# Kernel optimization log

Hardware: AMD Instinct MI355X
Metric: run time of the kernel (lower is better)

## Reference

```python
import jax, jax.numpy as jnp
import numpy as np

VOCAB, EMB = 50000, 300
HID, FCH = 128, 64
B, T = 1024, 200


def setup_inputs() -> dict:
    key = jax.random.key(0)
    ks = jax.random.split(key, 10)
    s = 0.05
    return {
        "x": jax.random.randint(ks[0], (B, T), 0, VOCAB),
        "emb_table": jax.random.normal(ks[1], (VOCAB, EMB), jnp.float32) * s,
        "w_ih": jax.random.normal(ks[2], (4 * HID, EMB), jnp.float32) * s,
        "w_hh": jax.random.normal(ks[3], (4 * HID, HID), jnp.float32) * s,
        "b_ih": jax.random.normal(ks[4], (4 * HID,), jnp.float32) * s,
        "b_hh": jax.random.normal(ks[5], (4 * HID,), jnp.float32) * s,
        "fc1_w": jax.random.normal(ks[6], (FCH, HID), jnp.float32) * s,
        "fc1_b": jax.random.normal(ks[7], (FCH,), jnp.float32) * s,
        "fc2_w": jax.random.normal(ks[8], (1, FCH), jnp.float32) * s,
        "fc2_b": jax.random.normal(ks[9], (1,), jnp.float32) * s,
    }


def _lstm_last_h(e, w_ih, w_hh, b_ih, b_hh):
    # e: [B, T, E] -> final hidden state [B, H]
    b, t, _ = e.shape
    h_dim = w_hh.shape[1]
    # Precompute input projections for all timesteps: [T, B, 4H]
    xg = jnp.einsum('bte,ge->tbg', e, w_ih) + (b_ih + b_hh)

    def step(carry, xg_t):
        h, c = carry
        gates = xg_t + h @ w_hh.T  # [B, 4H]
        i, f, g, o = jnp.split(gates, 4, axis=-1)  # PyTorch gate order i,f,g,o
        i = jax.nn.sigmoid(i)
        f = jax.nn.sigmoid(f)
        g = jnp.tanh(g)
        o = jax.nn.sigmoid(o)
        c = f * c + i * g
        h = o * jnp.tanh(c)
        return (h, c), None

    h0 = jnp.zeros((b, h_dim), e.dtype)
    c0 = jnp.zeros((b, h_dim), e.dtype)
    (h_n, _), _ = jax.lax.scan(step, (h0, c0), xg)
    return h_n


def reference(x, emb_table, w_ih, w_hh, b_ih, b_hh, fc1_w, fc1_b, fc2_w, fc2_b):
    e = emb_table[x]  # [B, T, E]
    hn = _lstm_last_h(e, w_ih, w_hh, b_ih, b_hh)  # [B, H]
    # dropout is identity in eval mode
    h1 = jax.nn.relu(hn @ fc1_w.T + fc1_b)  # [B, FCH]
    logits = h1 @ fc2_w.T + fc2_b  # [B, 1]
    return jax.nn.sigmoid(logits)
```

## Files before the change

### kernel.cpp

```cpp
#include <hip/hip_runtime.h>
#include <hip/hip_bf16.h>
#include <stdint.h>

#define VOCAB 50000
#define EMB   300
#define EMBP  320
#define HID   128
#define NGATE 512
#define BATCH 1024
#define SEQ   200
#define ROWS  4
#define L2E   1.4426950408889634f

typedef __attribute__((ext_vector_type(8))) short short8;
typedef __attribute__((ext_vector_type(4))) float f32x4;

#define AS1 __attribute__((address_space(1)))
#define AS3 __attribute__((address_space(3)))

static __device__ __forceinline__ void gload_lds16(const void* g, void* s) {
  __builtin_amdgcn_global_load_lds((const AS1 uint32_t*)g, (AS3 uint32_t*)s, 16, 0, 0);
}

static __device__ __forceinline__ unsigned short f2bf(float f) {
  union { float f; unsigned u; } v; v.f = f;
  unsigned r = v.u + 0x7fffu + ((v.u >> 16) & 1u);
  return (unsigned short)(r >> 16);
}
static __device__ __forceinline__ float blo2f(unsigned u) {
  union { unsigned u; float f; } v; v.u = u << 16; return v.f;
}
static __device__ __forceinline__ float bhi2f(unsigned u) {
  union { unsigned u; float f; } v; v.u = u & 0xffff0000u; return v.f;
}
static __device__ __forceinline__ float sigmf(float x) {
  return __fdividef(1.0f, 1.0f + __expf(-x));
}
static __device__ __forceinline__ float sig2(float z) {
  return __builtin_amdgcn_rcpf(1.0f + __builtin_amdgcn_exp2f(-z));
}

__global__ void k_cvt_pad(const float* __restrict__ src, unsigned short* __restrict__ dst,
                          int rows, int sc, int dc, int perm, int smode) {
  int idx = blockIdx.x * blockDim.x + threadIdx.x;
  int cpr = dc >> 3;
  if (idx >= rows * cpr) return;
  int row = idx / cpr, k0 = (idx - row * cpr) * 8;
  float s = 1.0f;
  if (smode) s = ((row >> 7) == 2) ? (2.0f * L2E) : L2E;
  uint4 pack;
  unsigned short* v = (unsigned short*)&pack;
#pragma unroll
  for (int j = 0; j < 8; j++) {
    int k = k0 + j;
    v[j] = (k < sc) ? f2bf(src[(long)row * sc + k] * s) : (unsigned short)0;
  }
  int drow = perm ? ((row & 127) * 4 + (row >> 7)) : row;
  *(uint4*)(dst + (long)drow * dc + k0) = pack;
}

__global__ void k_bias(const float* __restrict__ a, const float* __restrict__ b,
                       float* __restrict__ o) {
  int i = blockIdx.x * blockDim.x + threadIdx.x;
  if (i < NGATE) {
    int g = i >> 7, hid = i & 127;
    float s = (g == 2) ? (2.0f * L2E) : L2E;
    o[hid * 4 + g] = (a[i] + b[i]) * s;
  }
}

__global__ __launch_bounds__(256) void k_xg_gemm(
    const int* __restrict__ x, const unsigned short* __restrict__ embb,
    const unsigned short* __restrict__ wihb, const float* __restrict__ biasp,
    unsigned short* __restrict__ xg) {
  __shared__ __align__(16) unsigned short Al[128 * 64];
  __shared__ __align__(16) unsigned short Bl[128 * 64];
  const int tid = threadIdx.x;
  const int lane = tid & 63;
  const int tile_n = blockIdx.x & 3, tile_m = blockIdx.x >> 2;
  const int t_idx = tile_m >> 3;
  const int b0 = (tile_m & 7) * 128;
  const int n0 = tile_n * 128;

  const int r0 = tid >> 3;
  const int sg = (tid & 7) ^ (r0 & 7);
  const unsigned short* asrc[4];
  const unsigned short* bsrc[4];
#pragma unroll
  for (int i = 0; i < 4; i++) {
    const int r = r0 + i * 32;
    const long ridx = x[(b0 + r) * SEQ + t_idx];
    asrc[i] = embb + ridx * EMBP + sg * 8;
    bsrc[i] = wihb + (long)(n0 + r) * EMBP + sg * 8;
  }

  const int wid = tid >> 6;
  const int wrow = wid >> 1, wcol = wid & 1;
  const char* Ar = (const char*)Al + (wrow * 64) * 128;
  const char* Br = (const char*)Bl + (wcol * 64) * 128;
  const int l15 = lane & 15, lgrp = lane >> 4;
  const int swz = (l15 & 7) << 4;

  f32x4 acc[4][4];
#pragma unroll
  for (int mt = 0; mt < 4; mt++)
#pragma unroll
    for (int nt = 0; nt < 4; nt++) acc[mt][nt] = (f32x4){0.f, 0.f, 0.f, 0.f};

  for (int ks = 0; ks < EMBP / 64; ks++) {
#pragma unroll
    for (int i = 0; i < 4; i++) {
      gload_lds16(asrc[i] + ks * 64, (char*)Al + tid * 16 + i * 4096);
      gload_lds16(bsrc[i] + ks * 64, (char*)Bl + tid * 16 + i * 4096);
    }
    __syncthreads();
#pragma unroll
    for (int kt = 0; kt < 2; kt++) {
      short8 af[4], bf[4];
#pragma unroll
      for (int mt = 0; mt < 4; mt++)
        af[mt] = *(const short8*)(Ar + (mt * 16 + l15) * 128 + ((kt * 64 + lgrp * 16) ^ swz));
#pragma unroll
      for (int nt = 0; nt < 4; nt++)
        bf[nt] = *(const short8*)(Br + (nt * 16 + l15) * 128 + ((kt * 64 + lgrp * 16) ^ swz));
#pragma unroll
      for (int mt = 0; mt < 4; mt++)
#pragma unroll
        for (int nt = 0; nt < 4; nt++)
          acc[mt][nt] = __builtin_amdgcn_mfma_f32_16x16x32_bf16(af[mt], bf[nt], acc[mt][nt], 0, 0, 0);
    }
    __syncthreads();
  }

  const int m_base = tile_m * 128 + wrow * 64;
  const int colg = n0 + wcol * 64 + l15;
  const int rsub = lgrp * 4;
  float bv[4];
#pragma unroll
  for (int nt = 0; nt < 4; nt++) bv[nt] = biasp[colg + nt * 16];
#pragma unroll
  for (int mt = 0; mt < 4; mt++)
#pragma unroll
    for (int nt = 0; nt < 4; nt++)
#pragma unroll
      for (int j = 0; j < 4; j++) {
        const long m = m_base + mt * 16 + rsub + j;
        xg[m * NGATE + colg + nt * 16] = f2bf(acc[mt][nt][j] + bv[nt]);
      }
}

__global__ __launch_bounds__(512, 2) void k_lstm(
    const unsigned short* __restrict__ xg, const unsigned short* __restrict__ whhb,
    float* __restrict__ hfin) {
  __shared__ __align__(16) unsigned short h_lds[2 * 4 * 128];
  __shared__ __align__(16) float scratch[8 * 256];
  const int tid = threadIdx.x;
  const int lane = tid & 63;
  const int wid = tid >> 6;
  const int b0 = blockIdx.x * ROWS;
  const int l15 = lane & 15;
  const int lgrp = lane >> 4;
  const int hid = wid * 16 + l15;

  short8 bfr[4][4];
#pragma unroll
  for (int g = 0; g < 4; g++)
#pragma unroll
    for (int kt = 0; kt < 4; kt++)
      bfr[g][kt] = *(const short8*)(whhb + (g * 128 + hid) * HID + kt * 32 + lgrp * 8);

  float* sw = scratch + wid * 256;

  float c_r = 0.0f, h_r = 0.0f;

  if (tid < 128) ((uint4*)h_lds)[tid] = make_uint4(0, 0, 0, 0);
  __syncthreads();

  const int ar = l15 & 3;
  int rdoff[4];
#pragma unroll
  for (int kt = 0; kt < 4; kt++)
    rdoff[kt] = ar * 256 + ((kt * 64 + lgrp * 16) ^ (ar << 5));
  const int hwoff = lgrp * 256 + ((2 * hid) ^ (lgrp << 5));
  const char* lb = (const char*)h_lds;

  const unsigned short* xbase = xg + ((long)(b0 + lgrp) * HID + hid) * 4;
  const long TSTEP = (long)BATCH * HID * 4;
  uint2 xA = *(const uint2*)xbase;
  uint2 xB = *(const uint2*)(xbase + TSTEP);
  const unsigned short* xnext = xbase + 2 * TSTEP;

#define STEP_BODY(XS, RB, WB, T)                                               \
  {                                                                            \
    short8 af[4];                                                              \
    _Pragma("unroll") for (int kt = 0; kt < 4; kt++)                           \
      af[kt] = *(const short8*)(lb + (RB) + rdoff[kt]);                        \
    f32x4 acc[4];                                                              \
    _Pragma("unroll") for (int g = 0; g < 4; g++)                              \
      acc[g] = (f32x4){0.f, 0.f, 0.f, 0.f};                                    \
    _Pragma("unroll") for (int kt = 0; kt < 4; kt++)                           \
      _Pragma("unroll") for (int g = 0; g < 4; g++)                            \
        acc[g] = __builtin_amdgcn_mfma_f32_16x16x32_bf16(af[kt], bfr[g][kt],   \
                                                         acc[g], 0, 0, 0);     \
    if (lane < 16) {                                                           \
      _Pragma("unroll") for (int g = 0; g < 4; g++)                            \
        *(f32x4*)(sw + g * 64 + lane * 4) = acc[g];                            \
    }                                                                          \
    asm volatile("s_waitcnt lgkmcnt(0)" ::: "memory");                         \
    const float xf0 = blo2f(XS.x), xf1 = bhi2f(XS.x);                          \
    const float xf2 = blo2f(XS.y), xf3 = bhi2f(XS.y);                          \
    if ((T) + 2 < SEQ) XS = *(const uint2*)xnext;                              \
    const float zi = sw[0 * 64 + l15 * 4 + lgrp] + xf0;                        \
    const float zf = sw[1 * 64 + l15 * 4 + lgrp] + xf1;                        \
    const float zg = sw[2 * 64 + l15 * 4 + lgrp] + xf2;                        \
    const float zo = sw[3 * 64 + l15 * 4 + lgrp] + xf3;                        \
    const float iv = sig2(zi);                                                 \
    const float fv = sig2(zf);                                                 \
    const float gv = 2.0f * sig2(zg) - 1.0f;                                   \
    const float ov = sig2(zo);                                                 \
    c_r = fv * c_r + iv * gv;                                                  \
    const float tc = 2.0f * sig2(c_r * (2.0f * L2E)) - 1.0f;                   \
    h_r = ov * tc;                                                             \
    *(unsigned short*)((char*)h_lds + (WB) + hwoff) = f2bf(h_r);               \
    asm volatile("s_waitcnt lgkmcnt(0)" ::: "memory");                         \
    __builtin_amdgcn_s_barrier();                                              \
    __builtin_amdgcn_sched_barrier(0);                                         \
  }

  for (int t = 0; t < SEQ; t += 2) {
    STEP_BODY(xA, 0, 1024, t);
    xnext += TSTEP;
    STEP_BODY(xB, 1024, 0, t + 1);
    xnext += TSTEP;
  }
#undef STEP_BODY

  hfin[(b0 + lgrp) * HID + hid] = h_r;
}

__global__ void k_head(const float* __restrict__ hfin,
                       const float* __restrict__ fc1w, const float* __restrict__ fc1b,
                       const float* __restrict__ fc2w, const float* __restrict__ fc2b,
                       float* __restrict__ out) {
  const int tid = threadIdx.x;
  const int lane = tid & 63;
  const int wid = tid >> 6;
  const int row = blockIdx.x * 4 + wid;
  const float* h = hfin + row * HID;
  const float* w = fc1w + lane * HID;
  float acc = 0.0f;
#pragma unroll
  for (int k = 0; k < HID; k += 4) {
    const f32x4 hv = *(const f32x4*)(h + k);
    const f32x4 wv = *(const f32x4*)(w + k);
    acc += hv[0] * wv[0] + hv[1] * wv[1] + hv[2] * wv[2] + hv[3] * wv[3];
  }
  const float h1 = fmaxf(acc + fc1b[lane], 0.0f);
  float v = h1 * fc2w[lane];
#pragma unroll
  for (int off = 32; off > 0; off >>= 1) v += __shfl_down(v, off, 64);
  if (lane == 0) out[row] = sigmf(v + fc2b[0]);
}

extern "C" void kernel_launch(void* const* d_in, const int* in_sizes, int n_in,
                              void* d_out, int out_size, void* d_ws, size_t ws_size,
                              hipStream_t stream) {
  const int*   x    = (const int*)d_in[0];
  const float* emb  = (const float*)d_in[1];
  const float* w_ih = (const float*)d_in[2];
  const float* w_hh = (const float*)d_in[3];
  const float* b_ih = (const float*)d_in[4];
  const float* b_hh = (const float*)d_in[5];
  const float* fc1w = (const float*)d_in[6];
  const float* fc1b = (const float*)d_in[7];
  const float* fc2w = (const float*)d_in[8];
  const float* fc2b = (const float*)d_in[9];
  float* out = (float*)d_out;
  char* ws = (char*)d_ws;

  unsigned short* embb = (unsigned short*)(ws + 0);
  unsigned short* wihb = (unsigned short*)(ws + 32000000);
  unsigned short* whhb = (unsigned short*)(ws + 32327680);
  float*          biasp= (float*)(ws + 32458752);
  float*          hfinp= (float*)(ws + 32460800);
  unsigned short* xgb  = (unsigned short*)(ws + 32985088);

  k_cvt_pad<<<dim3((VOCAB * (EMBP / 8) + 255) / 256), dim3(256), 0, stream>>>(emb, embb, VOCAB, EMB, EMBP, 0, 0);
  k_cvt_pad<<<dim3((NGATE * (EMBP / 8) + 255) / 256), dim3(256), 0, stream>>>(w_ih, wihb, NGATE, EMB, EMBP, 1, 1);
  k_cvt_pad<<<dim3((NGATE * (HID / 8) + 255) / 256), dim3(256), 0, stream>>>(w_hh, whhb, NGATE, HID, HID, 0, 1);
  k_bias<<<dim3(2), dim3(256), 0, stream>>>(b_ih, b_hh, biasp);
  k_xg_gemm<<<dim3(1600 * 4), dim3(256), 0, stream>>>(x, embb, wihb, biasp, xgb);
  k_lstm<<<dim3(BATCH / ROWS), dim3(512), 0, stream>>>(xgb, whhb, hfinp);
  k_head<<<dim3(256), dim3(256), 0, stream>>>(hfinp, fc1w, fc1b, fc2w, fc2b, out);
  (void)in_sizes; (void)n_in; (void)out_size; (void)ws_size;
}
```

Baseline: 300.9 us.

## Double-buffer xg GEMM LDS stages and remap LSTM to 2 rows per block

```diff
diff --git a/kernel.cpp b/kernel.cpp
--- a/kernel.cpp
+++ b/kernel.cpp
@@ -9,11 +9,12 @@
 #define NGATE 512
 #define BATCH 1024
 #define SEQ   200
-#define ROWS  4
+#define ROWS  2
 #define L2E   1.4426950408889634f
 
 typedef __attribute__((ext_vector_type(8))) short short8;
 typedef __attribute__((ext_vector_type(4))) float f32x4;
+typedef __attribute__((ext_vector_type(2))) float f32x2;
 
 #define AS1 __attribute__((address_space(1)))
 #define AS3 __attribute__((address_space(3)))
@@ -73,8 +74,8 @@
     const int* __restrict__ x, const unsigned short* __restrict__ embb,
     const unsigned short* __restrict__ wihb, const float* __restrict__ biasp,
     unsigned short* __restrict__ xg) {
-  __shared__ __align__(16) unsigned short Al[128 * 64];
-  __shared__ __align__(16) unsigned short Bl[128 * 64];
+  __shared__ __align__(16) unsigned short Al[2][128 * 64];
+  __shared__ __align__(16) unsigned short Bl[2][128 * 64];
   const int tid = threadIdx.x;
   const int lane = tid & 63;
   const int tile_n = blockIdx.x & 3, tile_m = blockIdx.x >> 2;
@@ -96,8 +97,6 @@
 
   const int wid = tid >> 6;
   const int wrow = wid >> 1, wcol = wid & 1;
-  const char* Ar = (const char*)Al + (wrow * 64) * 128;
-  const char* Br = (const char*)Bl + (wcol * 64) * 128;
   const int l15 = lane & 15, lgrp = lane >> 4;
   const int swz = (l15 & 7) << 4;
 
@@ -107,30 +106,39 @@
 #pragma unroll
     for (int nt = 0; nt < 4; nt++) acc[mt][nt] = (f32x4){0.f, 0.f, 0.f, 0.f};
 
-  for (int ks = 0; ks < EMBP / 64; ks++) {
-#pragma unroll
-    for (int i = 0; i < 4; i++) {
-      gload_lds16(asrc[i] + ks * 64, (char*)Al + tid * 16 + i * 4096);
-      gload_lds16(bsrc[i] + ks * 64, (char*)Bl + tid * 16 + i * 4096);
-    }
-    __syncthreads();
-#pragma unroll
-    for (int kt = 0; kt < 2; kt++) {
-      short8 af[4], bf[4];
-#pragma unroll
-      for (int mt = 0; mt < 4; mt++)
-        af[mt] = *(const short8*)(Ar + (mt * 16 + l15) * 128 + ((kt * 64 + lgrp * 16) ^ swz));
-#pragma unroll
-      for (int nt = 0; nt < 4; nt++)
-        bf[nt] = *(const short8*)(Br + (nt * 16 + l15) * 128 + ((kt * 64 + lgrp * 16) ^ swz));
-#pragma unroll
-      for (int mt = 0; mt < 4; mt++)
-#pragma unroll
-        for (int nt = 0; nt < 4; nt++)
-          acc[mt][nt] = __builtin_amdgcn_mfma_f32_16x16x32_bf16(af[mt], bf[nt], acc[mt][nt], 0, 0, 0);
-    }
-    __syncthreads();
-  }
+#define STAGE(KS, BUF)                                                         \
+  {                                                                            \
+    _Pragma("unroll") for (int i = 0; i < 4; i++) {                            \
+      gload_lds16(asrc[i] + (KS) * 64, (char*)Al + (BUF) * 16384 + tid * 16 + i * 4096); \
+      gload_lds16(bsrc[i] + (KS) * 64, (char*)Bl + (BUF) * 16384 + tid * 16 + i * 4096); \
+    }                                                                          \
+  }
+
+#define COMPUTE(BUF)                                                           \
+  {                                                                            \
+    const char* Ar = (const char*)Al + (BUF) * 16384 + (wrow * 64) * 128;      \
+    const char* Br = (const char*)Bl + (BUF) * 16384 + (wcol * 64) * 128;      \
+    _Pragma("unroll") for (int kt = 0; kt < 2; kt++) {                         \
+      short8 af[4], bf[4];                                                     \
+      _Pragma("unroll") for (int mt = 0; mt < 4; mt++)                         \
+        af[mt] = *(const short8*)(Ar + (mt * 16 + l15) * 128 + ((kt * 64 + lgrp * 16) ^ swz)); \
+      _Pragma("unroll") for (int nt = 0; nt < 4; nt++)                         \
+        bf[nt] = *(const short8*)(Br + (nt * 16 + l15) * 128 + ((kt * 64 + lgrp * 16) ^ swz)); \
+      _Pragma("unroll") for (int mt = 0; mt < 4; mt++)                         \
+        _Pragma("unroll") for (int nt = 0; nt < 4; nt++)                       \
+          acc[mt][nt] = __builtin_amdgcn_mfma_f32_16x16x32_bf16(af[mt], bf[nt], acc[mt][nt], 0, 0, 0); \
+    }                                                                          \
+  }
+
+  STAGE(0, 0);
+  __syncthreads();
+  STAGE(1, 1); COMPUTE(0); __syncthreads();
+  STAGE(2, 0); COMPUTE(1); __syncthreads();
+  STAGE(3, 1); COMPUTE(0); __syncthreads();
+  STAGE(4, 0); COMPUTE(1); __syncthreads();
+  COMPUTE(0);
+#undef STAGE
+#undef COMPUTE
 
   const int m_base = tile_m * 128 + wrow * 64;
   const int colg = n0 + wcol * 64 + l15;
@@ -149,42 +157,51 @@
       }
 }
 
-__global__ __launch_bounds__(512, 2) void k_lstm(
+__global__ __launch_bounds__(256, 2) void k_lstm(
     const unsigned short* __restrict__ xg, const unsigned short* __restrict__ whhb,
     float* __restrict__ hfin) {
-  __shared__ __align__(16) unsigned short h_lds[2 * 4 * 128];
-  __shared__ __align__(16) float scratch[8 * 256];
+  __shared__ __align__(16) unsigned short h_lds[2 * 2 * 128];
+  __shared__ __align__(16) float scratch[4 * 256];
   const int tid = threadIdx.x;
   const int lane = tid & 63;
   const int wid = tid >> 6;
   const int b0 = blockIdx.x * ROWS;
   const int l15 = lane & 15;
   const int lgrp = lane >> 4;
-  const int hid = wid * 16 + l15;
-
-  short8 bfr[4][4];
-#pragma unroll
-  for (int g = 0; g < 4; g++)
+  const int brow = lane >> 5;
+  const int hidloc = lane & 31;
+  const int hid = wid * 32 + hidloc;
+
+  short8 bfr[8][4];
+#pragma unroll
+  for (int nt = 0; nt < 8; nt++) {
+    const int col = wid * 32 + (nt & 1) * 16 + l15;
+    const int g = nt >> 1;
 #pragma unroll
     for (int kt = 0; kt < 4; kt++)
-      bfr[g][kt] = *(const short8*)(whhb + (g * 128 + hid) * HID + kt * 32 + lgrp * 8);
-
+      bfr[nt][kt] = *(const short8*)(whhb + (g * 128 + col) * HID + kt * 32 + lgrp * 8);
+  }
+
+  float c_r = 0.0f, h_r = 0.0f;
+
+  ((unsigned*)h_lds)[tid] = 0;
+  __syncthreads();
+
+  int rdoff[4];
+#pragma unroll
+  for (int kt = 0; kt < 4; kt++)
+    rdoff[kt] = (l15 & 1) * 256 + kt * 64 + lgrp * 16;
+  const int hwoff = brow * 256 + hid * 2;
   float* sw = scratch + wid * 256;
-
-  float c_r = 0.0f, h_r = 0.0f;
-
-  if (tid < 128) ((uint4*)h_lds)[tid] = make_uint4(0, 0, 0, 0);
-  __syncthreads();
-
-  const int ar = l15 & 3;
-  int rdoff[4];
-#pragma unroll
-  for (int kt = 0; kt < 4; kt++)
-    rdoff[kt] = ar * 256 + ((kt * 64 + lgrp * 16) ^ (ar << 5));
-  const int hwoff = lgrp * 256 + ((2 * hid) ^ (lgrp << 5));
+  int swoff[8];
+#pragma unroll
+  for (int nt = 0; nt < 8; nt++)
+    swoff[nt] = (nt >> 1) * 64 + (nt & 1) * 32 + l15 * 2;
+  const int rd0 = hidloc * 2 + brow;
   const char* lb = (const char*)h_lds;
-
-  const unsigned short* xbase = xg + ((long)(b0 + lgrp) * HID + hid) * 4;
+  const f32x4 Z4 = (f32x4){0.f, 0.f, 0.f, 0.f};
+
+  const unsigned short* xbase = xg + ((long)(b0 + brow) * HID + hid) * 4;
   const long TSTEP = (long)BATCH * HID * 4;
   uint2 xA = *(const uint2*)xbase;
   uint2 xB = *(const uint2*)(xbase + TSTEP);
@@ -192,28 +209,27 @@
 
 #define STEP_BODY(XS, RB, WB, T)                                               \
   {                                                                            \
+    const float xf0 = blo2f(XS.x), xf1 = bhi2f(XS.x);                          \
+    const float xf2 = blo2f(XS.y), xf3 = bhi2f(XS.y);                          \
+    if ((T) + 2 < SEQ) XS = *(const uint2*)xnext;                              \
     short8 af[4];                                                              \
     _Pragma("unroll") for (int kt = 0; kt < 4; kt++)                           \
       af[kt] = *(const short8*)(lb + (RB) + rdoff[kt]);                        \
-    f32x4 acc[4];                                                              \
-    _Pragma("unroll") for (int g = 0; g < 4; g++)                              \
-      acc[g] = (f32x4){0.f, 0.f, 0.f, 0.f};                                    \
-    _Pragma("unroll") for (int kt = 0; kt < 4; kt++)                           \
-      _Pragma("unroll") for (int g = 0; g < 4; g++)                            \
-        acc[g] = __builtin_amdgcn_mfma_f32_16x16x32_bf16(af[kt], bfr[g][kt],   \
-                                                         acc[g], 0, 0, 0);     \
+    f32x4 acc[8];                                                              \
+    _Pragma("unroll") for (int nt = 0; nt < 8; nt++)                           \
+      acc[nt] = __builtin_amdgcn_mfma_f32_16x16x32_bf16(af[0], bfr[nt][0], Z4, 0, 0, 0); \
+    _Pragma("unroll") for (int kt = 1; kt < 4; kt++)                           \
+      _Pragma("unroll") for (int nt = 0; nt < 8; nt++)                         \
+        acc[nt] = __builtin_amdgcn_mfma_f32_16x16x32_bf16(af[kt], bfr[nt][kt], acc[nt], 0, 0, 0); \
     if (lane < 16) {                                                           \
-      _Pragma("unroll") for (int g = 0; g < 4; g++)                            \
-        *(f32x4*)(sw + g * 64 + lane * 4) = acc[g];                            \
+      _Pragma("unroll") for (int nt = 0; nt < 8; nt++)                         \
+        *(f32x2*)(sw + swoff[nt]) = (f32x2){acc[nt][0], acc[nt][1]};           \
     }                                                                          \
     asm volatile("s_waitcnt lgkmcnt(0)" ::: "memory");                         \
-    const float xf0 = blo2f(XS.x), xf1 = bhi2f(XS.x);                          \
-    const float xf2 = blo2f(XS.y), xf3 = bhi2f(XS.y);                          \
-    if ((T) + 2 < SEQ) XS = *(const uint2*)xnext;                              \
-    const float zi = sw[0 * 64 + l15 * 4 + lgrp] + xf0;                        \
-    const float zf = sw[1 * 64 + l15 * 4 + lgrp] + xf1;                        \
-    const float zg = sw[2 * 64 + l15 * 4 + lgrp] + xf2;                        \
-    const float zo = sw[3 * 64 + l15 * 4 + lgrp] + xf3;                        \
+    const float zi = sw[0 * 64 + rd0] + xf0;                                   \
+    const float zf = sw[1 * 64 + rd0] + xf1;                                   \
+    const float zg = sw[2 * 64 + rd0] + xf2;                                   \
+    const float zo = sw[3 * 64 + rd0] + xf3;                                   \
     const float iv = sig2(zi);                                                 \
     const float fv = sig2(zf);                                                 \
     const float gv = 2.0f * sig2(zg) - 1.0f;                                   \
@@ -228,14 +244,14 @@
   }
 
   for (int t = 0; t < SEQ; t += 2) {
-    STEP_BODY(xA, 0, 1024, t);
+    STEP_BODY(xA, 0, 512, t);
     xnext += TSTEP;
-    STEP_BODY(xB, 1024, 0, t + 1);
+    STEP_BODY(xB, 512, 0, t + 1);
     xnext += TSTEP;
   }
 #undef STEP_BODY
 
-  hfin[(b0 + lgrp) * HID + hid] = h_r;
+  hfin[(b0 + brow) * HID + hid] = h_r;
 }
 
 __global__ void k_head(const float* __restrict__ hfin,
@@ -290,7 +306,7 @@
   k_cvt_pad<<<dim3((NGATE * (HID / 8) + 255) / 256), dim3(256), 0, stream>>>(w_hh, whhb, NGATE, HID, HID, 0, 1);
   k_bias<<<dim3(2), dim3(256), 0, stream>>>(b_ih, b_hh, biasp);
   k_xg_gemm<<<dim3(1600 * 4), dim3(256), 0, stream>>>(x, embb, wihb, biasp, xgb);
-  k_lstm<<<dim3(BATCH / ROWS), dim3(512), 0, stream>>>(xgb, whhb, hfinp);
+  k_lstm<<<dim3(BATCH / ROWS), dim3(256), 0, stream>>>(xgb, whhb, hfinp);
   k_head<<<dim3(256), dim3(256), 0, stream>>>(hfinp, fc1w, fc1b, fc2w, fc2b, out);
   (void)in_sizes; (void)n_in; (void)out_size; (void)ws_size;
 }
```

After: 331.3 us. 1.1x slower.
